# Optimization experiments

Measured on AMD Instinct MI355X. Metric: run time of the kernel, lower is better.

The kernel has to match this reference:

```python
import jax, jax.numpy as jnp
import numpy as np

N = 50000
E = 800000
IN_C, HID, OUT_C, HEADS = 128, 32, 64, 4
NEG_SLOPE = 0.2


def setup_inputs() -> dict:
    key = jax.random.key(0)
    ks = jax.random.split(key, 10)
    x = jax.random.normal(ks[0], (N, IN_C), dtype=jnp.float32)
    edge_index = jax.random.randint(ks[1], (2, E), 0, N, dtype=jnp.int64)
    s = 0.05
    W1 = jax.random.normal(ks[2], (IN_C, HID), dtype=jnp.float32) * s
    b1 = jnp.zeros((HID,), dtype=jnp.float32)
    Wg = jax.random.normal(ks[3], (HID, HEADS * HID), dtype=jnp.float32) * s
    ag_src = jax.random.normal(ks[4], (HEADS, HID), dtype=jnp.float32) * s
    ag_dst = jax.random.normal(ks[5], (HEADS, HID), dtype=jnp.float32) * s
    bg = jnp.zeros((HID,), dtype=jnp.float32)
    W2 = jax.random.normal(ks[6], (HID, OUT_C), dtype=jnp.float32) * s
    b2 = jnp.zeros((OUT_C,), dtype=jnp.float32)
    return {"x": x, "edge_index": edge_index, "W1": W1, "b1": b1,
            "Wg": Wg, "ag_src": ag_src, "ag_dst": ag_dst, "bg": bg,
            "W2": W2, "b2": b2}


def _add_self_loops(edge_index, n):
    loop = jnp.arange(n, dtype=edge_index.dtype)
    return jnp.concatenate([edge_index, jnp.stack([loop, loop])], axis=1)


def _gcn(x, src, dst, W, b, n):
    # PyG GCNConv: symmetric normalization with self-loops, scatter-add
    xw = x @ W  # [N, F]
    deg = jnp.zeros((n,), xw.dtype).at[dst].add(1.0)  # in-degree incl self-loops
    dinv = jax.lax.rsqrt(deg)
    norm = dinv[src] * dinv[dst]  # [E']
    msg = xw[src] * norm[:, None]  # [E', F]
    out = jax.ops.segment_sum(msg, dst, num_segments=n)
    return out + b


def _gat(x, src, dst, Wg, a_src, a_dst, b, n):
    # PyG GATConv, concat=False (mean over heads), leaky_relu slope 0.2
    h = (x @ Wg).reshape(n, HEADS, HID)  # [N, H, D]
    al_s = jnp.einsum('nhd,hd->nh', h, a_src)  # [N, H]
    al_d = jnp.einsum('nhd,hd->nh', h, a_dst)
    logits = jax.nn.leaky_relu(al_s[src] + al_d[dst], NEG_SLOPE)  # [E', H]
    # segment softmax over incoming edges of each dst node
    m = jax.ops.segment_max(logits, dst, num_segments=n)
    e = jnp.exp(logits - m[dst])
    denom = jax.ops.segment_sum(e, dst, num_segments=n)
    alpha = e / denom[dst]  # [E', H]
    msg = h[src] * alpha[:, :, None]  # [E', H, D]
    out = jax.ops.segment_sum(msg, dst, num_segments=n)  # [N, H, D]
    return out.mean(axis=1) + b


def reference(x, edge_index, W1, b1, Wg, ag_src, ag_dst, bg, W2, b2):
    ei = _add_self_loops(edge_index, N)
    src, dst = ei[0], ei[1]
    h = jax.nn.relu(_gcn(x, src, dst, W1, b1, N))
    h = jax.nn.relu(_gat(h, src, dst, Wg, ag_src, ag_dst, bg, N))
    return _gcn(h, src, dst, W2, b2, N)
```

## Files before the change

### kernel.cpp

```cpp
#include <hip/hip_runtime.h>
#include <hip/hip_bf16.h>

#define N_NODES 50000
#define N_EDGES 800000
#define EP (N_EDGES + N_NODES)
#define IN_C 128
#define HID 32
#define OUT_C 64
#define HEADS 4
#define NEG_SLOPE 0.2f

#define NPB 128
#define K_BUCKETS ((N_NODES + NPB - 1) / NPB)

typedef unsigned int uint32;

__device__ __forceinline__ float bf_lo(uint32 u) { return __uint_as_float(u << 16); }
__device__ __forceinline__ float bf_hi(uint32 u) { return __uint_as_float(u & 0xffff0000u); }
__device__ __forceinline__ uint32 f2bf(float f) {
    uint32 u = __float_as_uint(f);
    return (u + 0x7fffu + ((u >> 16) & 1u)) >> 16;
}
__device__ __forceinline__ uint32 pack_bf2(float a, float b) {
    return f2bf(a) | (f2bf(b) << 16);
}

__global__ __launch_bounds__(512) void k_init2(int* __restrict__ gcnt,
                                               const float* __restrict__ Wg,
                                               const float* __restrict__ ags,
                                               const float* __restrict__ agd,
                                               float* __restrict__ wals,
                                               float* __restrict__ wald,
                                               const float* __restrict__ W2,
                                               uint32* __restrict__ wgp,
                                               uint32* __restrict__ w2p) {
    int t = threadIdx.x;
    if (t < K_BUCKETS + 1) gcnt[t] = 0;
    if (t < 256) {
        int c = t & 127;
        int h = c >> 5, k = c & 31;
        const float* a = (t < 128) ? ags : agd;
        float acc = 0.f;
#pragma unroll
        for (int d = 0; d < 32; d++) acc += Wg[k * 128 + h * 32 + d] * a[h * 32 + d];
        if (t < 128) wals[c] = acc; else wald[c] = acc;
    }
    for (int i = t; i < 2048; i += 512) {
        int j4 = i >> 6, d = (i >> 1) & 31, pp = i & 1;
        int c0 = 4 * j4 + 2 * pp, c1 = c0 + 1;
        float a = Wg[(c0 & 31) * 128 + (c0 >> 5) * 32 + d];
        float b = Wg[(c1 & 31) * 128 + (c1 >> 5) * 32 + d];
        wgp[i] = pack_bf2(a, b);
    }
    for (int i = t; i < 1024; i += 512) {
        int k4 = i >> 7, d = (i >> 1) & 63, pp = i & 1;
        int r0 = 4 * k4 + 2 * pp, r1 = r0 + 1;
        w2p[i] = pack_bf2(W2[r0 * 64 + d], W2[r1 * 64 + d]);
    }
}


__global__ __launch_bounds__(256) void k_bcount(const int* __restrict__ ei,
                                                int* __restrict__ gcnt) {
    __shared__ int h[K_BUCKETS];
    int t = threadIdx.x;
    for (int i = t; i < K_BUCKETS; i += 256) h[i] = 0;
    __syncthreads();
    int base = blockIdx.x * 4096;
    int dd[16];
#pragma unroll
    for (int k = 0; k < 16; k++) {
        int e = base + k * 256 + t;
        dd[k] = (e < N_EDGES) ? ei[N_EDGES + e] : -1;
    }
#pragma unroll
    for (int k = 0; k < 16; k++)
        if (dd[k] >= 0) atomicAdd(&h[dd[k] >> 7], 1);
    __syncthreads();
    for (int i = t; i < K_BUCKETS; i += 256)
        if (h[i]) atomicAdd(&gcnt[i], h[i]);
}

__global__ __launch_bounds__(512) void k_bscan(const int* __restrict__ gcnt,
                                               int* __restrict__ gbase,
                                               int* __restrict__ gcursor) {
    __shared__ int sd[512];
    int t = threadIdx.x;
    int v = (t < K_BUCKETS) ? gcnt[t] : 0;
    sd[t] = v;
    __syncthreads();
    for (int off = 1; off < 512; off <<= 1) {
        int x = (t >= off) ? sd[t - off] : 0;
        __syncthreads();
        sd[t] += x;
        __syncthreads();
    }
    if (t < K_BUCKETS) {
        int excl = sd[t] - v;
        gbase[t] = excl;
        gcursor[t] = excl;
    }
    if (t == 0) gbase[K_BUCKETS] = sd[K_BUCKETS - 1];
}

__global__ __launch_bounds__(256) void k_bucket(const int* __restrict__ ei,
                                                int* __restrict__ gcursor,
                                                uint32* __restrict__ gpairs) {
    __shared__ int cnt[K_BUCKETS];
    __shared__ int bas[K_BUCKETS];
    int t = threadIdx.x;
    for (int i = t; i < K_BUCKETS; i += 256) cnt[i] = 0;
    __syncthreads();
    int base = blockIdx.x * 2048;
    int ss[8], dd[8], ml[8];
#pragma unroll
    for (int k = 0; k < 8; k++) {
        int e = base + k * 256 + t;
        ss[k] = (e < N_EDGES) ? ei[e] : -1;
        dd[k] = (e < N_EDGES) ? ei[N_EDGES + e] : 0;
    }
#pragma unroll
    for (int k = 0; k < 8; k++)
        if (ss[k] >= 0) ml[k] = atomicAdd(&cnt[dd[k] >> 7], 1);
    __syncthreads();
    for (int i = t; i < K_BUCKETS; i += 256)
        bas[i] = cnt[i] ? atomicAdd(&gcursor[i], cnt[i]) : 0;
    __syncthreads();
#pragma unroll
    for (int k = 0; k < 8; k++)
        if (ss[k] >= 0)
            gpairs[bas[dd[k] >> 7] + ml[k]] = ((uint32)ss[k] << 7) | (uint32)(dd[k] & 127);
}

__global__ __launch_bounds__(256) void k_node(const uint32* __restrict__ gpairs,
                                              const int* __restrict__ gbase,
                                              int* __restrict__ offs,
                                              float* __restrict__ dinv,
                                              int* __restrict__ srcs) {
    __shared__ int cnt[NPB];
    __shared__ int scn[NPB];
    __shared__ int cur[NPB];
    int t = threadIdx.x;
    int b = blockIdx.x;
    int lo = b << 7;
    int nn = N_NODES - lo; if (nn > NPB) nn = NPB;
    int pb = gbase[b], pe = gbase[b + 1];
    if (t < NPB) cnt[t] = 0;
    __syncthreads();
    for (int i = pb + t; i < pe; i += 256)
        atomicAdd(&cnt[gpairs[i] & 127], 1);
    __syncthreads();
    if (t < NPB) scn[t] = cnt[t];
    __syncthreads();
    for (int off = 1; off < NPB; off <<= 1) {
        int x = 0;
        if (t >= off && t < NPB) x = scn[t - off];
        __syncthreads();
        if (t < NPB) scn[t] += x;
        __syncthreads();
    }
    if (t < nn) {
        int excl = scn[t] - cnt[t];
        int o = pb + excl + lo + t;
        offs[lo + t] = o;
        cur[t] = o;
        dinv[lo + t] = rsqrtf((float)(cnt[t] + 1));
        srcs[pb + scn[t] + lo + t] = lo + t;
    }
    if (b == K_BUCKETS - 1 && t == 0) offs[N_NODES] = pe + N_NODES;
    __syncthreads();
    for (int i = pb + t; i < pe; i += 256) {
        uint32 u = gpairs[i];
        int pos = atomicAdd(&cur[u & 127], 1);
        srcs[pos] = (int)(u >> 7);
    }
}

__global__ __launch_bounds__(256) void k_gemm1(const float* __restrict__ x,
                                               const float* __restrict__ W1,
                                               const float* __restrict__ dinv,
                                               uint32* __restrict__ xw1) {
    __shared__ float wl[IN_C * HID];
    __shared__ float xl[8 * IN_C];
    int t = threadIdx.x;
    for (int i = t; i < IN_C * HID; i += 256) {
        int k = i >> 5, f = i & 31;
        wl[(k >> 1) * 64 + f * 2 + (k & 1)] = W1[i];
    }
    int nb = blockIdx.x * 8;
    const float4* x4 = (const float4*)(x + (size_t)nb * IN_C);
    ((float4*)xl)[t] = x4[t];
    __syncthreads();
    int g = t >> 5, f = t & 31;
    const float2* xr = (const float2*)(xl + g * IN_C);
    const float2* wp = (const float2*)wl;
    float acc = 0.f;
#pragma unroll 16
    for (int k2 = 0; k2 < 64; k2++) {
        float2 xv = xr[k2];
        float2 wv = wp[k2 * 32 + f];
        acc += xv.x * wv.x + xv.y * wv.y;
    }
    float v = acc * dinv[nb + g];
    float vn = __shfl_xor(v, 1, 64);
    if ((f & 1) == 0) xw1[(size_t)(nb + g) * 16 + (f >> 1)] = pack_bf2(v, vn);
}

__global__ __launch_bounds__(256) void k_gather1(const uint32* __restrict__ xw1,
                                                 const int* __restrict__ offs,
                                                 const int* __restrict__ srcs,
                                                 const float* __restrict__ dinv,
                                                 const float* __restrict__ b1,
                                                 const float* __restrict__ wals,
                                                 const float* __restrict__ wald,
                                                 char* __restrict__ rec) {
    int t = threadIdx.x;
    int l16 = t & 15;
    int n = blockIdx.x * 16 + (t >> 4);
    int s0 = offs[n], s1 = offs[n + 1];
    const char* xb = (const char*)xw1 + l16 * 4;
    float a0 = 0.f, a1 = 0.f, a2 = 0.f, a3 = 0.f;
    int j = s0;
    for (; j + 1 < s1; j += 2) {
        uint32 uA = *(const uint32*)(xb + ((uint32)srcs[j] << 6));
        uint32 uB = *(const uint32*)(xb + ((uint32)srcs[j + 1] << 6));
        a0 += bf_lo(uA); a1 += bf_hi(uA);
        a2 += bf_lo(uB); a3 += bf_hi(uB);
    }
    if (j < s1) {
        uint32 uA = *(const uint32*)(xb + ((uint32)srcs[j] << 6));
        a0 += bf_lo(uA); a1 += bf_hi(uA);
    }
    float dn = dinv[n];
    float2 b = ((const float2*)b1)[l16];
    float vx = (a0 + a2) * dn + b.x;
    float vy = (a1 + a3) * dn + b.y;
    vx = vx > 0.f ? vx : 0.f;
    vy = vy > 0.f ? vy : 0.f;
    char* rn = rec + (size_t)n * 128;
    *(uint32*)(rn + 64 + l16 * 4) = pack_bf2(vx, vy);

    float ps0, ps1, ps2, ps3, pd0, pd1, pd2, pd3;
    {
        float2 w0 = ((const float2*)wals)[0 * 16 + l16];
        float2 w1 = ((const float2*)wals)[1 * 16 + l16];
        float2 w2 = ((const float2*)wals)[2 * 16 + l16];
        float2 w3 = ((const float2*)wals)[3 * 16 + l16];
        ps0 = vx * w0.x + vy * w0.y;
        ps1 = vx * w1.x + vy * w1.y;
        ps2 = vx * w2.x + vy * w2.y;
        ps3 = vx * w3.x + vy * w3.y;
        float2 u0 = ((const float2*)wald)[0 * 16 + l16];
        float2 u1 = ((const float2*)wald)[1 * 16 + l16];
        float2 u2 = ((const float2*)wald)[2 * 16 + l16];
        float2 u3 = ((const float2*)wald)[3 * 16 + l16];
        pd0 = vx * u0.x + vy * u0.y;
        pd1 = vx * u1.x + vy * u1.y;
        pd2 = vx * u2.x + vy * u2.y;
        pd3 = vx * u3.x + vy * u3.y;
    }
#pragma unroll
    for (int m = 1; m < 16; m <<= 1) {
        ps0 += __shfl_xor(ps0, m, 16); ps1 += __shfl_xor(ps1, m, 16);
        ps2 += __shfl_xor(ps2, m, 16); ps3 += __shfl_xor(ps3, m, 16);
        pd0 += __shfl_xor(pd0, m, 16); pd1 += __shfl_xor(pd1, m, 16);
        pd2 += __shfl_xor(pd2, m, 16); pd3 += __shfl_xor(pd3, m, 16);
    }
    if (l16 == 0) {
        float4* r4 = (float4*)rn;
        r4[0] = make_float4(__expf(ps0), __expf(ps1), __expf(ps2), __expf(ps3));
        r4[1] = make_float4(__expf(NEG_SLOPE * ps0), __expf(NEG_SLOPE * ps1),
                            __expf(NEG_SLOPE * ps2), __expf(NEG_SLOPE * ps3));
        r4[2] = make_float4(__expf(pd0), __expf(pd1), __expf(pd2), __expf(pd3));
        r4[3] = make_float4(__expf(NEG_SLOPE * pd0), __expf(NEG_SLOPE * pd1),
                            __expf(NEG_SLOPE * pd2), __expf(NEG_SLOPE * pd3));
    }
}

__global__ __launch_bounds__(256) void k_gat_agg(const char* __restrict__ rec,
                                                 const int* __restrict__ offs,
                                                 const int* __restrict__ srcs,
                                                 const uint32* __restrict__ wgp,
                                                 const float* __restrict__ bg,
                                                 const float* __restrict__ dinv,
                                                 uint32* __restrict__ h2s) {
    __shared__ __align__(16) uint32 wl[2048];
    __shared__ __align__(16) uint32 gl[8][64];
    int t = threadIdx.x;
    {
        const uint4* src4 = (const uint4*)wgp;
        uint4* dst4 = (uint4*)wl;
        dst4[t] = src4[t];
        dst4[256 + t] = src4[256 + t];
    }

    int l32 = t & 31;
    int g8 = t >> 5;
    int n = blockIdx.x * 8 + g8;
    int l16 = l32 & 15;
    int par = l32 >> 4;
    int s0 = offs[n], s1 = offs[n + 1];
    const float4* dn4 = (const float4*)(rec + (size_t)n * 128);
    float4 d1 = dn4[2];
    float4 d2 = dn4[3];
    uint32 hoff = 64 + l16 * 4;

    float g00 = 0.f, g01 = 0.f, g10 = 0.f, g11 = 0.f;
    float g20 = 0.f, g21 = 0.f, g30 = 0.f, g31 = 0.f;
    float ss0 = 0.f, ss1 = 0.f, ss2 = 0.f, ss3 = 0.f;

#define GAT_EDGE(J)                                                            \
    {                                                                          \
        uint32 off = (uint32)srcs[J] << 7;                                     \
        float4 e1 = *(const float4*)(rec + off);                               \
        float4 e2 = *(const float4*)(rec + off + 16);                          \
        uint32 u = *(const uint32*)(rec + off + hoff);                         \
        float flo = bf_lo(u), fhi = bf_hi(u);                                  \
        float p, q, w;                                                         \
        p = e1.x * d1.x; q = e2.x * d2.x; w = p > 1.f ? p : q;                 \
        ss0 += w; g00 += w * flo; g01 += w * fhi;                              \
        p = e1.y * d1.y; q = e2.y * d2.y; w = p > 1.f ? p : q;                 \
        ss1 += w; g10 += w * flo; g11 += w * fhi;                              \
        p = e1.z * d1.z; q = e2.z * d2.z; w = p > 1.f ? p : q;                 \
        ss2 += w; g20 += w * flo; g21 += w * fhi;                              \
        p = e1.w * d1.w; q = e2.w * d2.w; w = p > 1.f ? p : q;                 \
        ss3 += w; g30 += w * flo; g31 += w * fhi;                              \
    }

    int j = s0 + par;
    for (; j + 2 < s1; j += 4) {
        GAT_EDGE(j);
        GAT_EDGE(j + 2);
    }
    if (j < s1) GAT_EDGE(j);
#undef GAT_EDGE

    ss0 += __shfl_xor(ss0, 16, 64); ss1 += __shfl_xor(ss1, 16, 64);
    ss2 += __shfl_xor(ss2, 16, 64); ss3 += __shfl_xor(ss3, 16, 64);
    g00 += __shfl_xor(g00, 16, 64); g01 += __shfl_xor(g01, 16, 64);
    g10 += __shfl_xor(g10, 16, 64); g11 += __shfl_xor(g11, 16, 64);
    g20 += __shfl_xor(g20, 16, 64); g21 += __shfl_xor(g21, 16, 64);
    g30 += __shfl_xor(g30, 16, 64); g31 += __shfl_xor(g31, 16, 64);
    float i0 = 0.25f / ss0, i1 = 0.25f / ss1, i2 = 0.25f / ss2, i3 = 0.25f / ss3;
    if (l32 < 16) {
        gl[g8][0 * 16 + l16] = pack_bf2(g00 * i0, g01 * i0);
        gl[g8][1 * 16 + l16] = pack_bf2(g10 * i1, g11 * i1);
        gl[g8][2 * 16 + l16] = pack_bf2(g20 * i2, g21 * i2);
        gl[g8][3 * 16 + l16] = pack_bf2(g30 * i3, g31 * i3);
    }
    __syncthreads();
    const uint2* gv = (const uint2*)gl[g8];
    const uint2* wp = (const uint2*)wl;
    int d = l32;
    float acc = 0.f;
#pragma unroll 8
    for (int j4 = 0; j4 < 32; j4++) {
        uint2 gg = gv[j4];
        uint2 ww = wp[j4 * 32 + d];
        acc += bf_lo(gg.x) * bf_lo(ww.x) + bf_hi(gg.x) * bf_hi(ww.x)
             + bf_lo(gg.y) * bf_lo(ww.y) + bf_hi(gg.y) * bf_hi(ww.y);
    }
    float v = acc + bg[d];
    v = v > 0.f ? v : 0.f;
    v *= dinv[n];
    float vn = __shfl_xor(v, 1, 64);
    if ((d & 1) == 0) h2s[(size_t)n * 16 + (d >> 1)] = pack_bf2(v, vn);
}

__global__ __launch_bounds__(256) void k_gather2(const uint32* __restrict__ h2s,
                                                 const int* __restrict__ offs,
                                                 const int* __restrict__ srcs,
                                                 const uint32* __restrict__ w2p,
                                                 const float* __restrict__ dinv,
                                                 const float* __restrict__ b2,
                                                 float* __restrict__ out) {
    __shared__ __align__(16) uint32 wl[1024];
    __shared__ __align__(16) uint32 gbf[16][16];
    int t = threadIdx.x;
    ((uint4*)wl)[t] = ((const uint4*)w2p)[t];

    int l16 = t & 15;
    int g16 = t >> 4;
    int n = blockIdx.x * 16 + g16;
    int s0 = offs[n], s1 = offs[n + 1];
    const char* xb = (const char*)h2s + l16 * 4;
    float a0 = 0.f, a1 = 0.f, a2 = 0.f, a3 = 0.f;
    int j = s0;
    for (; j + 1 < s1; j += 2) {
        uint32 uA = *(const uint32*)(xb + ((uint32)srcs[j] << 6));
        uint32 uB = *(const uint32*)(xb + ((uint32)srcs[j + 1] << 6));
        a0 += bf_lo(uA); a1 += bf_hi(uA);
        a2 += bf_lo(uB); a3 += bf_hi(uB);
    }
    if (j < s1) {
        uint32 uA = *(const uint32*)(xb + ((uint32)srcs[j] << 6));
        a0 += bf_lo(uA); a1 += bf_hi(uA);
    }
    gbf[g16][l16] = pack_bf2(a0 + a2, a1 + a3);
    __syncthreads();
    const uint2* gv = (const uint2*)gbf[g16];
    const uint2* wp = (const uint2*)wl;
    float dn = dinv[n];
    float acc0 = 0.f, acc1 = 0.f, acc2 = 0.f, acc3 = 0.f;
#pragma unroll
    for (int k4 = 0; k4 < 8; k4++) {
        uint2 gg = gv[k4];
        float gx = bf_lo(gg.x), gy = bf_hi(gg.x);
        float gz = bf_lo(gg.y), gw = bf_hi(gg.y);
        uint2 w0 = wp[k4 * 64 + l16];
        uint2 w1 = wp[k4 * 64 + l16 + 16];
        uint2 w2 = wp[k4 * 64 + l16 + 32];
        uint2 w3 = wp[k4 * 64 + l16 + 48];
        acc0 += gx * bf_lo(w0.x) + gy * bf_hi(w0.x) + gz * bf_lo(w0.y) + gw * bf_hi(w0.y);
        acc1 += gx * bf_lo(w1.x) + gy * bf_hi(w1.x) + gz * bf_lo(w1.y) + gw * bf_hi(w1.y);
        acc2 += gx * bf_lo(w2.x) + gy * bf_hi(w2.x) + gz * bf_lo(w2.y) + gw * bf_hi(w2.y);
        acc3 += gx * bf_lo(w3.x) + gy * bf_hi(w3.x) + gz * bf_lo(w3.y) + gw * bf_hi(w3.y);
    }
    float* op = out + (size_t)n * OUT_C;
    op[l16]      = acc0 * dn + b2[l16];
    op[l16 + 16] = acc1 * dn + b2[l16 + 16];
    op[l16 + 32] = acc2 * dn + b2[l16 + 32];
    op[l16 + 48] = acc3 * dn + b2[l16 + 48];
}

extern "C" void kernel_launch(void* const* d_in, const int* in_sizes, int n_in,
                              void* d_out, int out_size, void* d_ws, size_t ws_size,
                              hipStream_t stream) {
    const float* x   = (const float*)d_in[0];
    const int*   ei  = (const int*)d_in[1];
    const float* W1  = (const float*)d_in[2];
    const float* b1  = (const float*)d_in[3];
    const float* Wg  = (const float*)d_in[4];
    const float* ags = (const float*)d_in[5];
    const float* agd = (const float*)d_in[6];
    const float* bg  = (const float*)d_in[7];
    const float* W2  = (const float*)d_in[8];
    const float* b2  = (const float*)d_in[9];
    float* out = (float*)d_out;

    char* p = (char*)d_ws;
    auto alloc = [&](size_t bytes) -> void* {
        void* r = (void*)p;
        p += (bytes + 255) & ~(size_t)255;
        return r;
    };
    float*  dinv    = (float*)alloc((size_t)N_NODES * 4);
    int*    offs    = (int*)  alloc((size_t)(N_NODES + 1) * 4);
    int*    gcnt    = (int*)  alloc((size_t)(K_BUCKETS + 1) * 4);
    int*    gbase   = (int*)  alloc((size_t)(K_BUCKETS + 1) * 4);
    int*    gcursor = (int*)  alloc((size_t)(K_BUCKETS + 1) * 4);
    int*    srcs    = (int*)  alloc((size_t)EP * 4);
    uint32* gpairs  = (uint32*)alloc((size_t)N_EDGES * 4);
    uint32* xw1     = (uint32*)alloc((size_t)N_NODES * 16 * 4);
    char*   rec     = (char*) alloc((size_t)N_NODES * 128);
    float*  wals    = (float*)alloc(128 * 4);
    float*  wald    = (float*)alloc(128 * 4);
    uint32* wgp     = (uint32*)alloc(2048 * 4);
    uint32* w2p     = (uint32*)alloc(1024 * 4);
    uint32* h2s     = (uint32*)alloc((size_t)N_NODES * 16 * 4);

    k_init2<<<1, 512, 0, stream>>>(gcnt, Wg, ags, agd, wals, wald, W2, wgp, w2p);
    k_bcount<<<(N_EDGES + 4095) / 4096, 256, 0, stream>>>(ei, gcnt);
    k_bscan<<<1, 512, 0, stream>>>(gcnt, gbase, gcursor);
    k_bucket<<<(N_EDGES + 2047) / 2048, 256, 0, stream>>>(ei, gcursor, gpairs);
    k_node<<<K_BUCKETS, 256, 0, stream>>>(gpairs, gbase, offs, dinv, srcs);

    k_gemm1<<<N_NODES / 8, 256, 0, stream>>>(x, W1, dinv, xw1);
    k_gather1<<<N_NODES / 16, 256, 0, stream>>>(xw1, offs, srcs, dinv, b1,
                                                wals, wald, rec);

    k_gat_agg<<<N_NODES / 8, 256, 0, stream>>>(rec, offs, srcs, wgp, bg, dinv, h2s);

    k_gather2<<<N_NODES / 16, 256, 0, stream>>>(h2s, offs, srcs, w2p, dinv, b2, out);
}
```

Before: 233.3 us.

## Use MFMA bf16 for post-aggregation projections in GAT and final GCN kernels

Replaces the scalar per-thread dot products that apply Wg and W2 after aggregation with 16x16x32 bf16 MFMA instructions. The weights are prepacked into the MFMA B-fragment layout in the init kernel, and the per-block LDS copies of the weights are removed. The GAT kernel now handles 16 nodes per 512-thread block so one wave can do an MFMA tile. The cost is that only one wave per block does the matmul while the others wait, and fragment loads come straight from global memory.

After: 218.2 us. -6.5%, faster.

```diff
diff --git a/kernel.cpp b/kernel.cpp
--- a/kernel.cpp
+++ b/kernel.cpp
@@ -14,6 +14,8 @@
 #define K_BUCKETS ((N_NODES + NPB - 1) / NPB)
 
 typedef unsigned int uint32;
+typedef __attribute__((ext_vector_type(8))) short bf16x8;
+typedef __attribute__((ext_vector_type(4))) float f32x4;
 
 __device__ __forceinline__ float bf_lo(uint32 u) { return __uint_as_float(u << 16); }
 __device__ __forceinline__ float bf_hi(uint32 u) { return __uint_as_float(u & 0xffff0000u); }
@@ -32,8 +34,8 @@
                                                float* __restrict__ wals,
                                                float* __restrict__ wald,
                                                const float* __restrict__ W2,
-                                               uint32* __restrict__ wgp,
-                                               uint32* __restrict__ w2p) {
+                                               uint32* __restrict__ wgB,
+                                               uint32* __restrict__ w2B) {
     int t = threadIdx.x;
     if (t < K_BUCKETS + 1) gcnt[t] = 0;
     if (t < 256) {
@@ -46,16 +48,24 @@
         if (t < 128) wals[c] = acc; else wald[c] = acc;
     }
     for (int i = t; i < 2048; i += 512) {
-        int j4 = i >> 6, d = (i >> 1) & 31, pp = i & 1;
-        int c0 = 4 * j4 + 2 * pp, c1 = c0 + 1;
-        float a = Wg[(c0 & 31) * 128 + (c0 >> 5) * 32 + d];
-        float b = Wg[(c1 & 31) * 128 + (c1 >> 5) * 32 + d];
-        wgp[i] = pack_bf2(a, b);
+        int tile = i >> 8;
+        int T = tile >> 2, kt = tile & 3;
+        int r = i & 255;
+        int L = r >> 2, di = r & 3;
+        int k0 = kt * 32 + (L >> 4) * 8 + 2 * di;
+        int k1 = k0 + 1;
+        int n = T * 16 + (L & 15);
+        float a = Wg[(k0 & 31) * 128 + (k0 >> 5) * 32 + n];
+        float b = Wg[(k1 & 31) * 128 + (k1 >> 5) * 32 + n];
+        wgB[i] = pack_bf2(a, b);
     }
     for (int i = t; i < 1024; i += 512) {
-        int k4 = i >> 7, d = (i >> 1) & 63, pp = i & 1;
-        int r0 = 4 * k4 + 2 * pp, r1 = r0 + 1;
-        w2p[i] = pack_bf2(W2[r0 * 64 + d], W2[r1 * 64 + d]);
+        int T = i >> 8;
+        int r = i & 255;
+        int L = r >> 2, di = r & 3;
+        int k0 = (L >> 4) * 8 + 2 * di;
+        int n = T * 16 + (L & 15);
+        w2B[i] = pack_bf2(W2[k0 * 64 + n], W2[(k0 + 1) * 64 + n]);
     }
 }
 
@@ -277,26 +287,18 @@
     }
 }
 
-__global__ __launch_bounds__(256) void k_gat_agg(const char* __restrict__ rec,
+__global__ __launch_bounds__(512) void k_gat_agg(const char* __restrict__ rec,
                                                  const int* __restrict__ offs,
                                                  const int* __restrict__ srcs,
-                                                 const uint32* __restrict__ wgp,
+                                                 const uint32* __restrict__ wgB,
                                                  const float* __restrict__ bg,
                                                  const float* __restrict__ dinv,
                                                  uint32* __restrict__ h2s) {
-    __shared__ __align__(16) uint32 wl[2048];
-    __shared__ __align__(16) uint32 gl[8][64];
-    int t = threadIdx.x;
-    {
-        const uint4* src4 = (const uint4*)wgp;
-        uint4* dst4 = (uint4*)wl;
-        dst4[t] = src4[t];
-        dst4[256 + t] = src4[256 + t];
-    }
-
+    __shared__ __align__(16) uint32 gl[16][64];
+    int t = threadIdx.x;
     int l32 = t & 31;
     int g8 = t >> 5;
-    int n = blockIdx.x * 8 + g8;
+    int n = blockIdx.x * 16 + g8;
     int l16 = l32 & 15;
     int par = l32 >> 4;
     int s0 = offs[n], s1 = offs[n + 1];
@@ -349,36 +351,50 @@
         gl[g8][3 * 16 + l16] = pack_bf2(g30 * i3, g31 * i3);
     }
     __syncthreads();
-    const uint2* gv = (const uint2*)gl[g8];
-    const uint2* wp = (const uint2*)wl;
-    int d = l32;
-    float acc = 0.f;
-#pragma unroll 8
-    for (int j4 = 0; j4 < 32; j4++) {
-        uint2 gg = gv[j4];
-        uint2 ww = wp[j4 * 32 + d];
-        acc += bf_lo(gg.x) * bf_lo(ww.x) + bf_hi(gg.x) * bf_hi(ww.x)
-             + bf_lo(gg.y) * bf_lo(ww.y) + bf_hi(gg.y) * bf_hi(ww.y);
-    }
-    float v = acc + bg[d];
-    v = v > 0.f ? v : 0.f;
-    v *= dinv[n];
-    float vn = __shfl_xor(v, 1, 64);
-    if ((d & 1) == 0) h2s[(size_t)n * 16 + (d >> 1)] = pack_bf2(v, vn);
+    if (t < 64) {
+        int L = t;
+        int mA = L & 15;
+        int quad = L >> 4;
+        int nbase = blockIdx.x * 16;
+        float dn0 = dinv[nbase + quad * 4 + 0];
+        float dn1 = dinv[nbase + quad * 4 + 1];
+        float dn2 = dinv[nbase + quad * 4 + 2];
+        float dn3 = dinv[nbase + quad * 4 + 3];
+#pragma unroll
+        for (int T = 0; T < 2; T++) {
+            f32x4 acc = {0.f, 0.f, 0.f, 0.f};
+#pragma unroll
+            for (int kt = 0; kt < 4; kt++) {
+                bf16x8 af = *(const bf16x8*)&gl[mA][kt * 16 + quad * 4];
+                bf16x8 bf = *(const bf16x8*)(wgB + (size_t)((T * 4 + kt) * 64 + L) * 4);
+                acc = __builtin_amdgcn_mfma_f32_16x16x32_bf16(af, bf, acc, 0, 0, 0);
+            }
+            int d = T * 16 + (L & 15);
+            float bgd = bg[d];
+            float dns[4] = {dn0, dn1, dn2, dn3};
+#pragma unroll
+            for (int r = 0; r < 4; r++) {
+                int node = nbase + quad * 4 + r;
+                float v = acc[r] + bgd;
+                v = v > 0.f ? v : 0.f;
+                v *= dns[r];
+                float vn = __shfl_xor(v, 1, 64);
+                if ((d & 1) == 0)
+                    h2s[(size_t)node * 16 + (d >> 1)] = pack_bf2(v, vn);
+            }
+        }
+    }
 }
 
 __global__ __launch_bounds__(256) void k_gather2(const uint32* __restrict__ h2s,
                                                  const int* __restrict__ offs,
                                                  const int* __restrict__ srcs,
-                                                 const uint32* __restrict__ w2p,
+                                                 const uint32* __restrict__ w2B,
                                                  const float* __restrict__ dinv,
                                                  const float* __restrict__ b2,
                                                  float* __restrict__ out) {
-    __shared__ __align__(16) uint32 wl[1024];
     __shared__ __align__(16) uint32 gbf[16][16];
     int t = threadIdx.x;
-    ((uint4*)wl)[t] = ((const uint4*)w2p)[t];
-
     int l16 = t & 15;
     int g16 = t >> 4;
     int n = blockIdx.x * 16 + g16;
@@ -398,29 +414,28 @@
     }
     gbf[g16][l16] = pack_bf2(a0 + a2, a1 + a3);
     __syncthreads();
-    const uint2* gv = (const uint2*)gbf[g16];
-    const uint2* wp = (const uint2*)wl;
-    float dn = dinv[n];
-    float acc0 = 0.f, acc1 = 0.f, acc2 = 0.f, acc3 = 0.f;
-#pragma unroll
-    for (int k4 = 0; k4 < 8; k4++) {
-        uint2 gg = gv[k4];
-        float gx = bf_lo(gg.x), gy = bf_hi(gg.x);
-        float gz = bf_lo(gg.y), gw = bf_hi(gg.y);
-        uint2 w0 = wp[k4 * 64 + l16];
-        uint2 w1 = wp[k4 * 64 + l16 + 16];
-        uint2 w2 = wp[k4 * 64 + l16 + 32];
-        uint2 w3 = wp[k4 * 64 + l16 + 48];
-        acc0 += gx * bf_lo(w0.x) + gy * bf_hi(w0.x) + gz * bf_lo(w0.y) + gw * bf_hi(w0.y);
-        acc1 += gx * bf_lo(w1.x) + gy * bf_hi(w1.x) + gz * bf_lo(w1.y) + gw * bf_hi(w1.y);
-        acc2 += gx * bf_lo(w2.x) + gy * bf_hi(w2.x) + gz * bf_lo(w2.y) + gw * bf_hi(w2.y);
-        acc3 += gx * bf_lo(w3.x) + gy * bf_hi(w3.x) + gz * bf_lo(w3.y) + gw * bf_hi(w3.y);
-    }
-    float* op = out + (size_t)n * OUT_C;
-    op[l16]      = acc0 * dn + b2[l16];
-    op[l16 + 16] = acc1 * dn + b2[l16 + 16];
-    op[l16 + 32] = acc2 * dn + b2[l16 + 32];
-    op[l16 + 48] = acc3 * dn + b2[l16 + 48];
+    if (t < 64) {
+        int L = t;
+        int quad = L >> 4;
+        int nbase = blockIdx.x * 16;
+        float dns[4];
+#pragma unroll
+        for (int r = 0; r < 4; r++) dns[r] = dinv[nbase + quad * 4 + r];
+        bf16x8 af = *(const bf16x8*)&gbf[L & 15][quad * 4];
+#pragma unroll
+        for (int T = 0; T < 4; T++) {
+            bf16x8 bf = *(const bf16x8*)(w2B + (size_t)(T * 64 + L) * 4);
+            f32x4 acc = {0.f, 0.f, 0.f, 0.f};
+            acc = __builtin_amdgcn_mfma_f32_16x16x32_bf16(af, bf, acc, 0, 0, 0);
+            int d = T * 16 + (L & 15);
+            float b2d = b2[d];
+#pragma unroll
+            for (int r = 0; r < 4; r++) {
+                int node = nbase + quad * 4 + r;
+                out[(size_t)node * OUT_C + d] = acc[r] * dns[r] + b2d;
+            }
+        }
+    }
 }
 
 extern "C" void kernel_launch(void* const* d_in, const int* in_sizes, int n_in,
@@ -455,11 +470,11 @@
     char*   rec     = (char*) alloc((size_t)N_NODES * 128);
     float*  wals    = (float*)alloc(128 * 4);
     float*  wald    = (float*)alloc(128 * 4);
-    uint32* wgp     = (uint32*)alloc(2048 * 4);
-    uint32* w2p     = (uint32*)alloc(1024 * 4);
+    uint32* wgB     = (uint32*)alloc(2048 * 4);
+    uint32* w2B     = (uint32*)alloc(1024 * 4);
     uint32* h2s     = (uint32*)alloc((size_t)N_NODES * 16 * 4);
 
-    k_init2<<<1, 512, 0, stream>>>(gcnt, Wg, ags, agd, wals, wald, W2, wgp, w2p);
+    k_init2<<<1, 512, 0, stream>>>(gcnt, Wg, ags, agd, wals, wald, W2, wgB, w2B);
     k_bcount<<<(N_EDGES + 4095) / 4096, 256, 0, stream>>>(ei, gcnt);
     k_bscan<<<1, 512, 0, stream>>>(gcnt, gbase, gcursor);
     k_bucket<<<(N_EDGES + 2047) / 2048, 256, 0, stream>>>(ei, gcursor, gpairs);
@@ -469,7 +484,7 @@
     k_gather1<<<N_NODES / 16, 256, 0, stream>>>(xw1, offs, srcs, dinv, b1,
                                                 wals, wald, rec);
 
-    k_gat_agg<<<N_NODES / 8, 256, 0, stream>>>(rec, offs, srcs, wgp, bg, dinv, h2s);
-
-    k_gather2<<<N_NODES / 16, 256, 0, stream>>>(h2s, offs, srcs, w2p, dinv, b2, out);
-}
+    k_gat_agg<<<N_NODES / 16, 512, 0, stream>>>(rec, offs, srcs, wgB, bg, dinv, h2s);
+
+    k_gather2<<<N_NODES / 16, 256, 0, stream>>>(h2s, offs, srcs, w2B, dinv, b2, out);
+}
```
